# Kernel optimization log

Hardware: AMD Instinct MI355X
Metric: run time of the kernel (lower is better)

## Reference

```python
import jax, jax.numpy as jnp
import numpy as np

B, N = 8, 4096
T_MAX = 100.0
NEG_INF = -1e20


def setup_inputs() -> dict:
    key = jax.random.key(0)
    k1, k2, k3, k4, k5 = jax.random.split(key, 5)
    # sorted event times in [0, T_MAX)
    event_times = jnp.sort(jax.random.uniform(k1, (B, N), dtype=jnp.float32) * T_MAX, axis=-1)
    input_mask = jnp.ones((B, N), dtype=jnp.float32)
    t0 = jnp.zeros((B,), dtype=jnp.float32)
    t1 = jnp.full((B,), T_MAX, dtype=jnp.float32)
    mu = jax.random.normal(k3, (1,), dtype=jnp.float32) * 0.1
    alpha = jax.random.normal(k4, (1,), dtype=jnp.float32) * 0.1
    beta = jax.random.normal(k5, (1,), dtype=jnp.float32) * 0.1
    return {"event_times": event_times, "input_mask": input_mask, "t0": t0, "t1": t1,
            "mu": mu, "alpha": alpha, "beta": beta}


def reference(event_times, input_mask, t0, t1, mu, alpha, beta):
    mu = jax.nn.softplus(mu)      # [1]
    alpha = jax.nn.softplus(alpha)
    beta = jax.nn.softplus(beta)
    # pairwise time differences: dt[b, i, j] = t_i - t_j
    dt = event_times[:, :, None] - event_times[:, None, :]          # [B, N, N]
    # fill_triu(-dt*beta, -1e20): keep only strictly-lower triangle (j < i)
    i_idx = jnp.arange(event_times.shape[-1])
    triu = i_idx[:, None] <= i_idx[None, :]                          # j >= i -> masked
    scores = jnp.where(triu, NEG_INF, -dt * beta)                    # [B, N, N]
    lamb = jnp.exp(jax.nn.logsumexp(scores, axis=-1)) * alpha * beta + mu  # [B, N]
    loglik = (jnp.log(lamb + 1e-8) * input_mask).sum(-1)             # [B]
    log_kernel = -beta * (t1[:, None] - event_times) * input_mask + (1.0 - input_mask) * NEG_INF
    compensator = (t1 - t0) * mu                                     # [B]
    compensator = compensator - alpha * (jnp.exp(jax.nn.logsumexp(log_kernel, axis=-1)) - input_mask.sum(-1))
    return loglik - compensator                                      # [B]
```

## Files before the change

kernel.cpp:

```cpp
#include <hip/hip_runtime.h>
#include <math.h>


#define NB 256
#define NN 4096
#define CC (NN / NB)
#define NW (NB / 64)

__global__ __launch_bounds__(NB) void hawkes_kernel(
    const float* __restrict__ T, const float* __restrict__ M,
    const float* __restrict__ t0, const float* __restrict__ t1,
    const float* __restrict__ mu, const float* __restrict__ alpha,
    const float* __restrict__ beta, float* __restrict__ out, int N)
{
    const int b    = blockIdx.x;
    const int tid  = threadIdx.x;
    const int lane = tid & 63;
    const int wv   = tid >> 6;

    __shared__ float sh_t[NN];
    __shared__ float wd[NW], ww[NW];
    __shared__ float red[3][NW];

    const float* Tb = T + (size_t)b * N;
    const float* Mb = M + (size_t)b * N;

    for (int i = tid; i < N; i += NB) sh_t[i] = Tb[i];
    __syncthreads();

    const float mu_s = log1pf(expf(mu[0]));
    const float al_s = log1pf(expf(alpha[0]));
    const float be_s = log1pf(expf(beta[0]));
    const float ab   = al_s * be_s;
    const float t1v  = t1[b];
    const float t0v  = t0[b];

    const int s = tid * CC;

    float within[CC], decay[CC];
    float w = 0.f, d = 1.f;
    float tprev = sh_t[s];
    within[0] = 0.f; decay[0] = 1.f;
    for (int k = 1; k < CC; ++k) {
        float ti = sh_t[s + k];
        float a  = expf(-be_s * (ti - tprev));
        w = a * (w + 1.f);
        d = d * a;
        within[k] = w; decay[k] = d;
        tprev = ti;
    }
    float D, W;
    if (s + CC < N) {
        float tn = sh_t[s + CC];
        float a  = expf(-be_s * (tn - tprev));
        W = a * (w + 1.f);
        D = d * a;
    } else { D = 0.f; W = 0.f; }

    float di = D, wi = W;
    for (int off = 1; off < 64; off <<= 1) {
        float dp = __shfl_up(di, off);
        float wp = __shfl_up(wi, off);
        if (lane >= off) { wi = di * wp + wi; di = di * dp; }
    }
    if (lane == 63) { wd[wv] = di; ww[wv] = wi; }
    __syncthreads();

    float cw = 0.f;
    for (int j = 0; j < wv; ++j) cw = wd[j] * cw + ww[j];

    float de = __shfl_up(di, 1);
    float we = __shfl_up(wi, 1);
    if (lane == 0) { de = 1.f; we = 0.f; }
    const float carry = de * cw + we;

    float ll = 0.f, ce = 0.f, ms = 0.f;
    for (int k = 0; k < CC; ++k) {
        int i = s + k;
        float ti = sh_t[i];
        float m  = Mb[i];
        float S  = decay[k] * carry + within[k];
        float lamb = ab * S + mu_s;
        ll += logf(lamb + 1e-8f) * m;
        float lk = -be_s * (t1v - ti) * m + (1.f - m) * (-1e20f);
        ce += expf(lk);
        ms += m;
    }

    for (int off = 32; off > 0; off >>= 1) {
        ll += __shfl_down(ll, off);
        ce += __shfl_down(ce, off);
        ms += __shfl_down(ms, off);
    }
    if (lane == 0) { red[0][wv] = ll; red[1][wv] = ce; red[2][wv] = ms; }
    __syncthreads();
    if (tid == 0) {
        float L = 0.f, C = 0.f, Msum = 0.f;
        for (int j = 0; j < NW; ++j) { L += red[0][j]; C += red[1][j]; Msum += red[2][j]; }
        float comp = (t1v - t0v) * mu_s - al_s * (C - Msum);
        out[b] = L - comp;
    }
}

extern "C" void kernel_launch(void* const* d_in, const int* in_sizes, int n_in,
                              void* d_out, int out_size, void* d_ws, size_t ws_size,
                              hipStream_t stream) {
    (void)n_in; (void)d_ws; (void)ws_size;
    const float* T     = (const float*)d_in[0];
    const float* M     = (const float*)d_in[1];
    const float* t0    = (const float*)d_in[2];
    const float* t1    = (const float*)d_in[3];
    const float* mu    = (const float*)d_in[4];
    const float* alpha = (const float*)d_in[5];
    const float* beta  = (const float*)d_in[6];
    float* out = (float*)d_out;

    const int B = in_sizes[2];
    const int N = in_sizes[0] / B;

    hawkes_kernel<<<B, NB, 0, stream>>>(T, M, t0, t1, mu, alpha, beta, out, N);
    (void)out_size;
}
```

Measured before the change: 69.07 us.

## Load chunks directly into registers with float4, precompute exps, use fast intrinsics

```diff
diff --git a/kernel.cpp b/kernel.cpp
--- a/kernel.cpp
+++ b/kernel.cpp
@@ -3,8 +3,7 @@
 
 
 #define NB 256
-#define NN 4096
-#define CC (NN / NB)
+#define CC 16
 #define NW (NB / 64)
 
 __global__ __launch_bounds__(NB) void hawkes_kernel(
@@ -18,15 +17,24 @@
     const int lane = tid & 63;
     const int wv   = tid >> 6;
 
-    __shared__ float sh_t[NN];
     __shared__ float wd[NW], ww[NW];
     __shared__ float red[3][NW];
 
     const float* Tb = T + (size_t)b * N;
     const float* Mb = M + (size_t)b * N;
+    const int s = tid * CC;
 
-    for (int i = tid; i < N; i += NB) sh_t[i] = Tb[i];
-    __syncthreads();
+    float t[CC], m[CC];
+    const float4* T4 = (const float4*)(Tb + s);
+    const float4* M4 = (const float4*)(Mb + s);
+#pragma unroll
+    for (int q = 0; q < CC / 4; ++q) {
+        float4 tv = T4[q], mv = M4[q];
+        t[4*q+0] = tv.x; t[4*q+1] = tv.y; t[4*q+2] = tv.z; t[4*q+3] = tv.w;
+        m[4*q+0] = mv.x; m[4*q+1] = mv.y; m[4*q+2] = mv.z; m[4*q+3] = mv.w;
+    }
+    const bool has_next = (s + CC < N);
+    const float tn = has_next ? Tb[s + CC] : 0.f;
 
     const float mu_s = log1pf(expf(mu[0]));
     const float al_s = log1pf(expf(alpha[0]));
@@ -35,29 +43,25 @@
     const float t1v  = t1[b];
     const float t0v  = t0[b];
 
-    const int s = tid * CC;
+    float a[CC];
+#pragma unroll
+    for (int k = 1; k < CC; ++k) a[k] = __expf(-be_s * (t[k] - t[k-1]));
+    const float aN = __expf(-be_s * (tn - t[CC-1]));
 
     float within[CC], decay[CC];
+    within[0] = 0.f; decay[0] = 1.f;
     float w = 0.f, d = 1.f;
-    float tprev = sh_t[s];
-    within[0] = 0.f; decay[0] = 1.f;
+#pragma unroll
     for (int k = 1; k < CC; ++k) {
-        float ti = sh_t[s + k];
-        float a  = expf(-be_s * (ti - tprev));
-        w = a * (w + 1.f);
-        d = d * a;
+        w = a[k] * (w + 1.f);
+        d = d * a[k];
         within[k] = w; decay[k] = d;
-        tprev = ti;
     }
-    float D, W;
-    if (s + CC < N) {
-        float tn = sh_t[s + CC];
-        float a  = expf(-be_s * (tn - tprev));
-        W = a * (w + 1.f);
-        D = d * a;
-    } else { D = 0.f; W = 0.f; }
+    float D = has_next ? d * aN        : 0.f;
+    float W = has_next ? aN * (w + 1.f): 0.f;
 
     float di = D, wi = W;
+#pragma unroll
     for (int off = 1; off < 64; off <<= 1) {
         float dp = __shfl_up(di, off);
         float wp = __shfl_up(wi, off);
@@ -74,19 +78,20 @@
     if (lane == 0) { de = 1.f; we = 0.f; }
     const float carry = de * cw + we;
 
-    float ll = 0.f, ce = 0.f, ms = 0.f;
+    float ll0 = 0.f, ll1 = 0.f, ce0 = 0.f, ce1 = 0.f, ms = 0.f;
+#pragma unroll
     for (int k = 0; k < CC; ++k) {
-        int i = s + k;
-        float ti = sh_t[i];
-        float m  = Mb[i];
-        float S  = decay[k] * carry + within[k];
-        float lamb = ab * S + mu_s;
-        ll += logf(lamb + 1e-8f) * m;
-        float lk = -be_s * (t1v - ti) * m + (1.f - m) * (-1e20f);
-        ce += expf(lk);
-        ms += m;
+        float S    = fmaf(decay[k], carry, within[k]);
+        float lamb = fmaf(ab, S, mu_s);
+        float lg   = __logf(lamb + 1e-8f) * m[k];
+        float lk   = fmaf(-be_s * (t1v - t[k]), m[k], (1.f - m[k]) * (-1e20f));
+        float ev   = __expf(lk);
+        if (k & 1) { ll1 += lg; ce1 += ev; } else { ll0 += lg; ce0 += ev; }
+        ms += m[k];
     }
+    float ll = ll0 + ll1, ce = ce0 + ce1;
 
+#pragma unroll
     for (int off = 32; off > 0; off >>= 1) {
         ll += __shfl_down(ll, off);
         ce += __shfl_down(ce, off);
@@ -105,7 +110,7 @@
 extern "C" void kernel_launch(void* const* d_in, const int* in_sizes, int n_in,
                               void* d_out, int out_size, void* d_ws, size_t ws_size,
                               hipStream_t stream) {
-    (void)n_in; (void)d_ws; (void)ws_size;
+    (void)n_in; (void)d_ws; (void)ws_size; (void)out_size;
     const float* T     = (const float*)d_in[0];
     const float* M     = (const float*)d_in[1];
     const float* t0    = (const float*)d_in[2];
@@ -119,5 +124,4 @@
     const int N = in_sizes[0] / B;
 
     hawkes_kernel<<<B, NB, 0, stream>>>(T, M, t0, t1, mu, alpha, beta, out, N);
-    (void)out_size;
 }
```

After: 66.37 us. 1.04x faster.
